# Optimization experiments

Hardware: AMD Instinct MI355X
Metric: run time of the kernel (lower is better)

## Reference

```python
import jax, jax.numpy as jnp
import numpy as np

D_MODEL = 128
REDUCTION = 4
KSIZE = 3
B = D_MODEL  # required by the original code's groups=B conv shape constraint
L = 4096


def setup_inputs() -> dict:
    key = jax.random.key(0)
    ks = jax.random.split(key, 7)
    d, r, K = D_MODEL, REDUCTION, KSIZE
    return {
        "x": jax.random.normal(ks[0], (B, L, d), dtype=jnp.float32),
        "W1": jax.random.normal(ks[1], (d // r, d), dtype=jnp.float32) * (1.0 / np.sqrt(d)),
        "b1": jax.random.normal(ks[2], (d // r,), dtype=jnp.float32) * 0.01,
        "W2": jax.random.normal(ks[3], (K, d // r), dtype=jnp.float32) * (1.0 / np.sqrt(d // r)),
        "b2": jax.random.normal(ks[4], (K,), dtype=jnp.float32) * 0.01,
        "Wc": jax.random.normal(ks[5], (d, d), dtype=jnp.float32) * (1.0 / np.sqrt(d)),
        "bc": jax.random.normal(ks[6], (d,), dtype=jnp.float32) * 0.01,
    }


def reference(x, W1, b1, W2, b2, Wc, bc):
    # x: [B, L, d] with B == d (required by original groups=B conv)
    Bsz, Lseq, d = x.shape
    K = W2.shape[0]
    pad = (K - 1) // 2
    # kernel generation from global average pool
    m = x.mean(axis=1)                                   # [B, d]
    h = jax.nn.gelu(m @ W1.T + b1, approximate=False)    # [B, d//r]
    w = jax.nn.softmax(h @ W2.T + b2, axis=-1)           # [B, K]; row j is the kernel for channel j
    # depthwise-style cross-correlation: y[b, l, c] = sum_k xp[b, l+k, c] * w[c, k]
    xp = jnp.pad(x, ((0, 0), (pad, pad), (0, 0)))        # [B, L+2*pad, d]
    y = sum(xp[:, k:k + Lseq, :] * w[None, None, :, k] for k in range(K))  # [B, L, d]
    # pointwise conv (kernel_size=1) == per-token linear
    return y @ Wc.T + bc                                 # [B, L, d]
```

## Files before the change

### kernel.cpp

```cpp
#include <hip/hip_runtime.h>
#include <hip/hip_bf16.h>

#define D_MODEL 128
#define SEQ_L   4096
#define BATCH   128
#define TM      64

typedef float f4 __attribute__((ext_vector_type(4)));
typedef float f32x4 __attribute__((ext_vector_type(4)));
typedef short bf16x8 __attribute__((ext_vector_type(8)));

__device__ __forceinline__ unsigned short f2bf(float f) {
    union { float f; unsigned u; } v; v.f = f;
    unsigned r = v.u + 0x7FFFu + ((v.u >> 16) & 1u);
    return (unsigned short)(r >> 16);
}

__global__ __launch_bounds__(256) void kmean(const float* __restrict__ x,
                                             float* __restrict__ part) {
    int seg = blockIdx.x, b = blockIdx.y;
    int t = threadIdx.x;
    int c4 = t & 31, ph = t >> 5;
    const f4* xb = reinterpret_cast<const f4*>(x + (size_t)b * SEQ_L * D_MODEL);
    int l0 = seg * 1024;
    f4 acc = {0.f, 0.f, 0.f, 0.f};
    for (int l = l0 + ph; l < l0 + 1024; l += 8)
        acc += xb[l * 32 + c4];
    __shared__ f4 red[256];
    red[t] = acc;
    __syncthreads();
    if (t < 32) {
        f4 s = red[t];
        #pragma unroll
        for (int p = 1; p < 8; ++p) s += red[t + 32 * p];
        reinterpret_cast<f4*>(part + ((size_t)b * 4 + seg) * D_MODEL)[t] = s;
    }
}

__global__ __launch_bounds__(128) void kweights(const float* __restrict__ part,
                                                const float* __restrict__ W1,
                                                const float* __restrict__ b1,
                                                const float* __restrict__ W2,
                                                const float* __restrict__ b2,
                                                float* __restrict__ w) {
    int c = threadIdx.x;
    const f4* p0 = reinterpret_cast<const f4*>(part + ((size_t)c * 4 + 0) * D_MODEL);
    const f4* p1 = reinterpret_cast<const f4*>(part + ((size_t)c * 4 + 1) * D_MODEL);
    const f4* p2 = reinterpret_cast<const f4*>(part + ((size_t)c * 4 + 2) * D_MODEL);
    const f4* p3 = reinterpret_cast<const f4*>(part + ((size_t)c * 4 + 3) * D_MODEL);
    f4 mv[32];
    #pragma unroll
    for (int d4 = 0; d4 < 32; ++d4)
        mv[d4] = (p0[d4] + p1[d4] + p2[d4] + p3[d4]) * (1.0f / (float)SEQ_L);

    float h[32];
    #pragma unroll
    for (int j = 0; j < 32; ++j) {
        const f4* w1r = reinterpret_cast<const f4*>(W1 + j * 128);
        f4 s4 = {0.f, 0.f, 0.f, 0.f};
        #pragma unroll
        for (int d4 = 0; d4 < 32; ++d4) s4 += mv[d4] * w1r[d4];
        float s = s4[0] + s4[1] + s4[2] + s4[3] + b1[j];
        h[j] = 0.5f * s * (1.0f + erff(s * 0.70710678118654752f));
    }
    float lg[3];
    float mx = -1e30f;
    #pragma unroll
    for (int k = 0; k < 3; ++k) {
        float s = b2[k];
        #pragma unroll
        for (int j = 0; j < 32; ++j) s += h[j] * W2[k * 32 + j];
        lg[k] = s;
        mx = fmaxf(mx, s);
    }
    float e[3], den = 0.f;
    #pragma unroll
    for (int k = 0; k < 3; ++k) { e[k] = __expf(lg[k] - mx); den += e[k]; }
    float inv = 1.0f / den;
    #pragma unroll
    for (int k = 0; k < 3; ++k) w[k * 128 + c] = e[k] * inv;
}

__global__ __launch_bounds__(256) void kcvt(const float* __restrict__ Wc,
                                            unsigned short* __restrict__ wcb) {
    int i = blockIdx.x * 256 + threadIdx.x;
    f4 v = reinterpret_cast<const f4*>(Wc)[i];
    ushort4 o;
    o.x = f2bf(v[0]); o.y = f2bf(v[1]); o.z = f2bf(v[2]); o.w = f2bf(v[3]);
    reinterpret_cast<ushort4*>(wcb)[i] = o;
}

__global__ __launch_bounds__(256) void kconv(const float* __restrict__ x,
                                             const float* __restrict__ w,
                                             const unsigned short* __restrict__ wcb,
                                             const float* __restrict__ bc,
                                             float* __restrict__ out) {
    __shared__ __align__(16) unsigned short y_lds[TM][136];
    __shared__ __align__(16) unsigned short wc_lds[128][136];

    int t = threadIdx.x;
    int b = blockIdx.y;
    int l0 = blockIdx.x * TM;
    const float* xb = x + (size_t)b * SEQ_L * D_MODEL;

    int c4 = t & 31;
    f4 w0 = reinterpret_cast<const f4*>(w)[c4];
    f4 w1 = reinterpret_cast<const f4*>(w + 128)[c4];
    f4 w2 = reinterpret_cast<const f4*>(w + 256)[c4];

    #pragma unroll
    for (int rp = 0; rp < 8; ++rp) {
        int r = (t >> 5) + rp * 8;
        int l = l0 + r;
        f4 xm = {0.f, 0.f, 0.f, 0.f}, xp = {0.f, 0.f, 0.f, 0.f};
        f4 x0 = reinterpret_cast<const f4*>(xb + (size_t)l * D_MODEL)[c4];
        if (l > 0)         xm = reinterpret_cast<const f4*>(xb + (size_t)(l - 1) * D_MODEL)[c4];
        if (l < SEQ_L - 1) xp = reinterpret_cast<const f4*>(xb + (size_t)(l + 1) * D_MODEL)[c4];
        f4 y = xm * w0 + x0 * w1 + xp * w2;
        ushort4 yb;
        yb.x = f2bf(y[0]); yb.y = f2bf(y[1]); yb.z = f2bf(y[2]); yb.w = f2bf(y[3]);
        *reinterpret_cast<ushort4*>(&y_lds[r][c4 * 4]) = yb;
    }

    {
        int row = t >> 4;
        int u8 = t & 15;
        #pragma unroll
        for (int p = 0; p < 8; ++p) {
            int rr = row + p * 16;
            uint4 v = reinterpret_cast<const uint4*>(wcb + (size_t)rr * 128)[u8];
            *reinterpret_cast<uint4*>(&wc_lds[rr][u8 * 8]) = v;
        }
    }
    __syncthreads();

    int lane = t & 63, wid = t >> 6;
    int m0 = wid * 16;
    int arow = m0 + (lane & 15);
    int kb = (lane >> 4) * 8;

    f32x4 acc[8];
    #pragma unroll
    for (int n = 0; n < 8; ++n) acc[n] = (f32x4){0.f, 0.f, 0.f, 0.f};

    #pragma unroll
    for (int kc = 0; kc < 4; ++kc) {
        bf16x8 a = *reinterpret_cast<const bf16x8*>(&y_lds[arow][kc * 32 + kb]);
        #pragma unroll
        for (int n = 0; n < 8; ++n) {
            bf16x8 bf = *reinterpret_cast<const bf16x8*>(&wc_lds[n * 16 + (lane & 15)][kc * 32 + kb]);
            acc[n] = __builtin_amdgcn_mfma_f32_16x16x32_bf16(a, bf, acc[n], 0, 0, 0);
        }
    }

    int colb = lane & 15;
    int rbase = m0 + (lane >> 4) * 4;
    #pragma unroll
    for (int n = 0; n < 8; ++n) {
        int co = n * 16 + colb;
        float bcv = bc[co];
        #pragma unroll
        for (int rr = 0; rr < 4; ++rr) {
            int l = l0 + rbase + rr;
            out[((size_t)b * SEQ_L + l) * D_MODEL + co] = acc[n][rr] + bcv;
        }
    }
}

extern "C" void kernel_launch(void* const* d_in, const int* in_sizes, int n_in,
                              void* d_out, int out_size, void* d_ws, size_t ws_size,
                              hipStream_t stream) {
    const float* x  = (const float*)d_in[0];
    const float* W1 = (const float*)d_in[1];
    const float* b1 = (const float*)d_in[2];
    const float* W2 = (const float*)d_in[3];
    const float* b2 = (const float*)d_in[4];
    const float* Wc = (const float*)d_in[5];
    const float* bc = (const float*)d_in[6];
    float* out = (float*)d_out;

    char* ws = (char*)d_ws;
    float* part = (float*)ws;
    float* w    = (float*)(ws + 262144);
    unsigned short* wcb = (unsigned short*)(ws + 264192);

    kmean<<<dim3(4, BATCH), 256, 0, stream>>>(x, part);
    kweights<<<1, 128, 0, stream>>>(part, W1, b1, W2, b2, w);
    kcvt<<<16, 256, 0, stream>>>(Wc, wcb);
    kconv<<<dim3(SEQ_L / TM, BATCH), 256, 0, stream>>>(x, w, wcb, bc, out);
}
```

Baseline: 281.1 us.

## Enlarge conv tile, reuse sliding x rows, swap MFMA operands for vector stores

Mean kernel now splits the sequence into 8 segments for more parallelism. The conv kernel uses 128-row tiles with 512 threads, and each thread walks 8 consecutive rows with a sliding window, so x rows are read once instead of three times. MFMA operands are swapped so each lane holds 4 consecutive output channels, which allows 16-byte vector stores instead of scalar strided stores. The larger tile increases LDS use per block and may reduce occupancy.

```diff
diff --git a/kernel.cpp b/kernel.cpp
--- a/kernel.cpp
+++ b/kernel.cpp
@@ -4,7 +4,8 @@
 #define D_MODEL 128
 #define SEQ_L   4096
 #define BATCH   128
-#define TM      64
+#define TM      128
+#define NSEG    8
 
 typedef float f4 __attribute__((ext_vector_type(4)));
 typedef float f32x4 __attribute__((ext_vector_type(4)));
@@ -22,9 +23,9 @@
     int t = threadIdx.x;
     int c4 = t & 31, ph = t >> 5;
     const f4* xb = reinterpret_cast<const f4*>(x + (size_t)b * SEQ_L * D_MODEL);
-    int l0 = seg * 1024;
+    int l0 = seg * (SEQ_L / NSEG);
     f4 acc = {0.f, 0.f, 0.f, 0.f};
-    for (int l = l0 + ph; l < l0 + 1024; l += 8)
+    for (int l = l0 + ph; l < l0 + SEQ_L / NSEG; l += 8)
         acc += xb[l * 32 + c4];
     __shared__ f4 red[256];
     red[t] = acc;
@@ -33,7 +34,7 @@
         f4 s = red[t];
         #pragma unroll
         for (int p = 1; p < 8; ++p) s += red[t + 32 * p];
-        reinterpret_cast<f4*>(part + ((size_t)b * 4 + seg) * D_MODEL)[t] = s;
+        reinterpret_cast<f4*>(part + ((size_t)b * NSEG + seg) * D_MODEL)[t] = s;
     }
 }
 
@@ -44,14 +45,16 @@
                                                 const float* __restrict__ b2,
                                                 float* __restrict__ w) {
     int c = threadIdx.x;
-    const f4* p0 = reinterpret_cast<const f4*>(part + ((size_t)c * 4 + 0) * D_MODEL);
-    const f4* p1 = reinterpret_cast<const f4*>(part + ((size_t)c * 4 + 1) * D_MODEL);
-    const f4* p2 = reinterpret_cast<const f4*>(part + ((size_t)c * 4 + 2) * D_MODEL);
-    const f4* p3 = reinterpret_cast<const f4*>(part + ((size_t)c * 4 + 3) * D_MODEL);
     f4 mv[32];
     #pragma unroll
-    for (int d4 = 0; d4 < 32; ++d4)
-        mv[d4] = (p0[d4] + p1[d4] + p2[d4] + p3[d4]) * (1.0f / (float)SEQ_L);
+    for (int d4 = 0; d4 < 32; ++d4) mv[d4] = (f4){0.f, 0.f, 0.f, 0.f};
+    for (int s = 0; s < NSEG; ++s) {
+        const f4* ps = reinterpret_cast<const f4*>(part + ((size_t)c * NSEG + s) * D_MODEL);
+        #pragma unroll
+        for (int d4 = 0; d4 < 32; ++d4) mv[d4] += ps[d4];
+    }
+    #pragma unroll
+    for (int d4 = 0; d4 < 32; ++d4) mv[d4] *= (1.0f / (float)SEQ_L);
 
     float h[32];
     #pragma unroll
@@ -90,11 +93,11 @@
     reinterpret_cast<ushort4*>(wcb)[i] = o;
 }
 
-__global__ __launch_bounds__(256) void kconv(const float* __restrict__ x,
-                                             const float* __restrict__ w,
-                                             const unsigned short* __restrict__ wcb,
-                                             const float* __restrict__ bc,
-                                             float* __restrict__ out) {
+__global__ __launch_bounds__(512, 4) void kconv(const float* __restrict__ x,
+                                                const float* __restrict__ w,
+                                                const unsigned short* __restrict__ wcb,
+                                                const float* __restrict__ bc,
+                                                float* __restrict__ out) {
     __shared__ __align__(16) unsigned short y_lds[TM][136];
     __shared__ __align__(16) unsigned short wc_lds[128][136];
 
@@ -108,35 +111,42 @@
     f4 w1 = reinterpret_cast<const f4*>(w + 128)[c4];
     f4 w2 = reinterpret_cast<const f4*>(w + 256)[c4];
 
-    #pragma unroll
-    for (int rp = 0; rp < 8; ++rp) {
-        int r = (t >> 5) + rp * 8;
-        int l = l0 + r;
-        f4 xm = {0.f, 0.f, 0.f, 0.f}, xp = {0.f, 0.f, 0.f, 0.f};
-        f4 x0 = reinterpret_cast<const f4*>(xb + (size_t)l * D_MODEL)[c4];
-        if (l > 0)         xm = reinterpret_cast<const f4*>(xb + (size_t)(l - 1) * D_MODEL)[c4];
-        if (l < SEQ_L - 1) xp = reinterpret_cast<const f4*>(xb + (size_t)(l + 1) * D_MODEL)[c4];
-        f4 y = xm * w0 + x0 * w1 + xp * w2;
-        ushort4 yb;
-        yb.x = f2bf(y[0]); yb.y = f2bf(y[1]); yb.z = f2bf(y[2]); yb.w = f2bf(y[3]);
-        *reinterpret_cast<ushort4*>(&y_lds[r][c4 * 4]) = yb;
+    {
+        int rg = t >> 5;
+        int r0 = rg * 8;
+        int lb = l0 + r0;
+        f4 prev = (lb > 0) ? reinterpret_cast<const f4*>(xb + (size_t)(lb - 1) * D_MODEL)[c4]
+                           : (f4){0.f, 0.f, 0.f, 0.f};
+        f4 cur = reinterpret_cast<const f4*>(xb + (size_t)lb * D_MODEL)[c4];
+        #pragma unroll
+        for (int i = 0; i < 8; ++i) {
+            int l = lb + i;
+            f4 nxt = (l < SEQ_L - 1)
+                         ? reinterpret_cast<const f4*>(xb + (size_t)(l + 1) * D_MODEL)[c4]
+                         : (f4){0.f, 0.f, 0.f, 0.f};
+            f4 y = prev * w0 + cur * w1 + nxt * w2;
+            ushort4 yb;
+            yb.x = f2bf(y[0]); yb.y = f2bf(y[1]); yb.z = f2bf(y[2]); yb.w = f2bf(y[3]);
+            *reinterpret_cast<ushort4*>(&y_lds[r0 + i][c4 * 4]) = yb;
+            prev = cur;
+            cur = nxt;
+        }
     }
 
     {
         int row = t >> 4;
-        int u8 = t & 15;
+        int u16 = t & 15;
         #pragma unroll
-        for (int p = 0; p < 8; ++p) {
-            int rr = row + p * 16;
-            uint4 v = reinterpret_cast<const uint4*>(wcb + (size_t)rr * 128)[u8];
-            *reinterpret_cast<uint4*>(&wc_lds[rr][u8 * 8]) = v;
+        for (int p = 0; p < 4; ++p) {
+            int rr = row + p * 32;
+            uint4 v = reinterpret_cast<const uint4*>(wcb + (size_t)rr * 128)[u16];
+            *reinterpret_cast<uint4*>(&wc_lds[rr][u16 * 8]) = v;
         }
     }
     __syncthreads();
 
     int lane = t & 63, wid = t >> 6;
-    int m0 = wid * 16;
-    int arow = m0 + (lane & 15);
+    int lrow = wid * 16 + (lane & 15);
     int kb = (lane >> 4) * 8;
 
     f32x4 acc[8];
@@ -145,25 +155,22 @@
 
     #pragma unroll
     for (int kc = 0; kc < 4; ++kc) {
-        bf16x8 a = *reinterpret_cast<const bf16x8*>(&y_lds[arow][kc * 32 + kb]);
+        bf16x8 by = *reinterpret_cast<const bf16x8*>(&y_lds[lrow][kc * 32 + kb]);
         #pragma unroll
         for (int n = 0; n < 8; ++n) {
-            bf16x8 bf = *reinterpret_cast<const bf16x8*>(&wc_lds[n * 16 + (lane & 15)][kc * 32 + kb]);
-            acc[n] = __builtin_amdgcn_mfma_f32_16x16x32_bf16(a, bf, acc[n], 0, 0, 0);
+            bf16x8 awc = *reinterpret_cast<const bf16x8*>(&wc_lds[n * 16 + (lane & 15)][kc * 32 + kb]);
+            acc[n] = __builtin_amdgcn_mfma_f32_16x16x32_bf16(awc, by, acc[n], 0, 0, 0);
         }
     }
 
-    int colb = lane & 15;
-    int rbase = m0 + (lane >> 4) * 4;
+    int l = l0 + wid * 16 + (lane & 15);
+    int cb = (lane >> 4) * 4;
+    float* orow = out + ((size_t)b * SEQ_L + l) * D_MODEL;
     #pragma unroll
     for (int n = 0; n < 8; ++n) {
-        int co = n * 16 + colb;
-        float bcv = bc[co];
-        #pragma unroll
-        for (int rr = 0; rr < 4; ++rr) {
-            int l = l0 + rbase + rr;
-            out[((size_t)b * SEQ_L + l) * D_MODEL + co] = acc[n][rr] + bcv;
-        }
+        f4 bcv = *reinterpret_cast<const f4*>(bc + n * 16 + cb);
+        f4 v = acc[n] + bcv;
+        *reinterpret_cast<f4*>(orow + n * 16 + cb) = v;
     }
 }
 
@@ -181,11 +188,11 @@
 
     char* ws = (char*)d_ws;
     float* part = (float*)ws;
-    float* w    = (float*)(ws + 262144);
-    unsigned short* wcb = (unsigned short*)(ws + 264192);
+    float* w    = (float*)(ws + 524288);
+    unsigned short* wcb = (unsigned short*)(ws + 526336);
 
-    kmean<<<dim3(4, BATCH), 256, 0, stream>>>(x, part);
+    kmean<<<dim3(NSEG, BATCH), 256, 0, stream>>>(x, part);
     kweights<<<1, 128, 0, stream>>>(part, W1, b1, W2, b2, w);
     kcvt<<<16, 256, 0, stream>>>(Wc, wcb);
-    kconv<<<dim3(SEQ_L / TM, BATCH), 256, 0, stream>>>(x, w, wcb, bc, out);
+    kconv<<<dim3(SEQ_L / TM, BATCH), 512, 0, stream>>>(x, w, wcb, bc, out);
 }
```

After: 264.5 us. 1.06x faster.
